# Kernel optimization log

Measured on AMD Instinct MI355X. Metric: run time of the kernel, lower is better.

## Reference

```python
import jax, jax.numpy as jnp
import numpy as np

B, T, D, H = 4, 2048, 512, 8
SCALE = np.float32(1.0 / np.sqrt(D))  # 'vaswani' scale, tied scalar, non-trainable
MASK_BIAS = np.float32(1e9)           # TF dense_attention masking constant


def setup_inputs() -> dict:
    key = jax.random.key(0)
    ks = jax.random.split(key, 5)
    s = 0.02  # small init so softmax logits are well-scaled
    return {
        "query": jax.random.normal(ks[0], (B, T, D), jnp.float32),
        "value": jax.random.normal(ks[1], (B, T, D), jnp.float32),
        "Wq": jax.random.normal(ks[2], (D, D * H), jnp.float32) * s,
        "bq": jnp.zeros((D * H,), jnp.float32),
        "Wk": jax.random.normal(ks[3], (D, D * H), jnp.float32) * s,
        "bk": jnp.zeros((D * H,), jnp.float32),
        "Wv": jax.random.normal(ks[4], (D, D * H), jnp.float32) * s,
        "bv": jnp.zeros((D * H,), jnp.float32),
    }


def reference(query, value, Wq, bq, Wk, bk, Wv, bv):
    # Per-head Dense projections (linear activation, depth=1): [B,T,D] -> [B,T,H*D]
    # split(axis=-1) into H heads + concat(axis=0) == reshape to [B,T,H,D]
    # (head h occupies contiguous slice [h*D:(h+1)*D] of the last axis)
    q = (query @ Wq + bq).reshape(B, T, H, D)
    k = (value @ Wk + bk).reshape(B, T, H, D)  # key defaults to value
    v = (value @ Wv + bv).reshape(B, T, H, D)
    # multiplicative scores: matmul(scale*q, k^T) -> [B,H,Tq,Tv]
    scores = jnp.einsum('bqhd,bkhd->bhqk', SCALE * q, k)
    # causal mask applied TF-style: scores -= 1e9 * (~mask)
    causal = jnp.tril(jnp.ones((T, T), bool))
    scores = jnp.where(causal, scores, scores - MASK_BIAS)
    attn = jax.nn.softmax(scores, axis=-1)          # [B,H,Tq,Tv]
    out = jnp.einsum('bhqk,bkhd->bqhd', attn, v)    # [B,Tq,H,D]
    # heads_output_mode='cat': concat heads back on feature axis
    return out.reshape(B, T, H * D)
```

## Files before the change

kernel.cpp:

```cpp
#include <hip/hip_runtime.h>
#include <stdint.h>

#define Bsz 4
#define Tsz 2048
#define Dsz 512
#define Hsz 8
#define HDsz 4096
#define Msz 8192
#define SCALE 0.044194173824159216f

typedef __attribute__((ext_vector_type(8))) short bf16x8;
typedef __attribute__((ext_vector_type(4))) float f32x4;
typedef __attribute__((ext_vector_type(4))) short s16x4;

static __device__ __forceinline__ short f2bf(float x) {
    uint32_t b = __float_as_uint(x);
    b += 0x7fff + ((b >> 16) & 1);
    return (short)(b >> 16);
}

__global__ __launch_bounds__(256) void xcast_kernel(
    const float* __restrict__ Xq, const float* __restrict__ Xv,
    short* __restrict__ Oq, short* __restrict__ Ov)
{
    int idx = blockIdx.x * 256 + threadIdx.x;
    const float* src = (idx < 1048576) ? Xq : Xv;
    short* dst = (idx < 1048576) ? Oq : Ov;
    int i = (idx < 1048576) ? idx : idx - 1048576;
    float4 v = *(const float4*)&src[(size_t)i * 4];
    s16x4 o;
    o.x = f2bf(v.x); o.y = f2bf(v.y); o.z = f2bf(v.z); o.w = f2bf(v.w);
    *(s16x4*)&dst[(size_t)i * 4] = o;
}

__global__ __launch_bounds__(256) void wtrans_kernel(
    const float* __restrict__ Wq, const float* __restrict__ Wk,
    const float* __restrict__ Wv, short* __restrict__ WtAll)
{
    const float* W = (blockIdx.z == 0) ? Wq : (blockIdx.z == 1) ? Wk : Wv;
    short* Wt = WtAll + (size_t)blockIdx.z * (size_t)HDsz * Dsz;
    __shared__ float tile[32][33];
    int tx = threadIdx.x, ty = threadIdx.y;
    int k0 = blockIdx.x * 32, n0 = blockIdx.y * 32;
    for (int i = 0; i < 4; i++)
        tile[ty + i * 8][tx] = W[(size_t)(k0 + ty + i * 8) * HDsz + n0 + tx];
    __syncthreads();
    for (int i = 0; i < 4; i++)
        Wt[(size_t)(n0 + ty + i * 8) * Dsz + k0 + tx] = f2bf(tile[tx][ty + i * 8]);
}

__global__ __launch_bounds__(256, 2) void proj_gemm_kernel(
    const short* __restrict__ Xqb, const short* __restrict__ Xvb,
    const short* __restrict__ WtAll, const float* __restrict__ bq,
    const float* __restrict__ bk, const float* __restrict__ bv,
    short* __restrict__ Qo, short* __restrict__ Ko, short* __restrict__ Vto)
{
    const int mode = blockIdx.z;
    const short* X = (mode == 0) ? Xqb : Xvb;
    const short* Wt = WtAll + (size_t)mode * (size_t)HDsz * Dsz;
    const float* bias = (mode == 0) ? bq : (mode == 1) ? bk : bv;
    const int m0 = blockIdx.x * 128, n0 = blockIdx.y * 128;

    __shared__ short Als[128 * 32];
    __shared__ short Bls[128 * 32];

    const int tid = threadIdx.x;
    const int lane = tid & 63, wave = tid >> 6;
    const int quad = lane >> 4, l16 = lane & 15;
    const int wm = wave >> 1, wn = wave & 1;

    const int dmarow = lane >> 2;
    const int dmachunk = (lane & 3) ^ ((lane >> 3) & 3);
    const int rdsw = (quad ^ ((l16 >> 1) & 3)) * 8;

    f32x4 acc[4][4];
    for (int i = 0; i < 4; i++)
        for (int j = 0; j < 4; j++)
            acc[i][j] = f32x4{0.f, 0.f, 0.f, 0.f};

    for (int ks = 0; ks < Dsz; ks += 32) {
        __syncthreads();
        for (int s = 0; s < 2; s++) {
            int c = wave * 2 + s;
            int row = c * 16 + dmarow;
            const short* ga = X + (size_t)(m0 + row) * Dsz + ks + dmachunk * 8;
            __builtin_amdgcn_global_load_lds(
                (const __attribute__((address_space(1))) void*)ga,
                (__attribute__((address_space(3))) void*)&Als[c * 512], 16, 0, 0);
            const short* gb = Wt + (size_t)(n0 + row) * Dsz + ks + dmachunk * 8;
            __builtin_amdgcn_global_load_lds(
                (const __attribute__((address_space(1))) void*)gb,
                (__attribute__((address_space(3))) void*)&Bls[c * 512], 16, 0, 0);
        }
        __syncthreads();
        bf16x8 af[4], bfr[4];
        for (int i = 0; i < 4; i++)
            af[i] = *(const bf16x8*)&Als[(wm * 64 + i * 16 + l16) * 32 + rdsw];
        for (int j = 0; j < 4; j++)
            bfr[j] = *(const bf16x8*)&Bls[(wn * 64 + j * 16 + l16) * 32 + rdsw];
        for (int i = 0; i < 4; i++)
            for (int j = 0; j < 4; j++)
                acc[i][j] = __builtin_amdgcn_mfma_f32_16x16x32_bf16(
                    af[i], bfr[j], acc[i][j], 0, 0, 0);
    }

    for (int i = 0; i < 4; i++) {
        for (int j = 0; j < 4; j++) {
            int n = n0 + wn * 64 + j * 16 + l16;
            int h = n >> 9, d = n & 511;
            float bb = bias[n];
            int mbase = m0 + wm * 64 + i * 16 + quad * 4;
            int b = mbase >> 11, t = mbase & 2047;
            if (mode == 2) {
                s16x4 o;
                o.x = f2bf(acc[i][j][0] + bb);
                o.y = f2bf(acc[i][j][1] + bb);
                o.z = f2bf(acc[i][j][2] + bb);
                o.w = f2bf(acc[i][j][3] + bb);
                *(s16x4*)&Vto[((size_t)(b * Hsz + h) * Dsz + d) * Tsz + t] = o;
            } else {
                short* O = (mode == 0) ? Qo : Ko;
                float sc = (mode == 0) ? SCALE : 1.0f;
                for (int r = 0; r < 4; r++) {
                    float v = (acc[i][j][r] + bb) * sc;
                    O[((size_t)(b * Hsz + h) * Tsz + (t + r)) * Dsz + d] = f2bf(v);
                }
            }
        }
    }
}

__global__ __launch_bounds__(512, 2) void attn_kernel(
    const short* __restrict__ Q, const short* __restrict__ K,
    const short* __restrict__ Vt, float* __restrict__ out)
{
    extern __shared__ short smem[];

    const int bid = blockIdx.x;
    const int qt = 15 - (bid >> 5);
    const int bh = bid & 31;
    const int q0 = qt * 128;
    const short* Qb = Q + (size_t)bh * Tsz * Dsz;
    const short* Kb = K + (size_t)bh * Tsz * Dsz;
    const short* Vb = Vt + (size_t)bh * Dsz * Tsz;

    const int tid = threadIdx.x;
    const int lane = tid & 63, wave = tid >> 6;
    const int quad = lane >> 4, l16 = lane & 15;
    const int qw = q0 + wave * 16;
    short* Pw = smem + 74240 + wave * (16 * 40);
    const int vrow = tid >> 2, vch = tid & 3;

    bf16x8 qf[16];
    for (int ks = 0; ks < 16; ks++)
        qf[ks] = *(const bf16x8*)&Qb[(size_t)(qw + l16) * Dsz + ks * 32 + quad * 8];

    f32x4 acc[32];
    for (int dt = 0; dt < 32; dt++) acc[dt] = f32x4{0.f, 0.f, 0.f, 0.f};
    float lacc[4] = {0.f, 0.f, 0.f, 0.f};

    {
        short* Ks0 = smem;
        short* Vs0 = smem + 33280;
        for (int i = 0; i < 4; i++) {
            int r = wave * 4 + i;
            const short* gp = Kb + (size_t)r * Dsz + lane * 8;
            __builtin_amdgcn_global_load_lds(
                (const __attribute__((address_space(1))) void*)gp,
                (__attribute__((address_space(3))) void*)&Ks0[r * 520], 16, 0, 0);
        }
        for (int p = 0; p < 4; p++) {
            int row = p * 128 + vrow;
            bf16x8 v = *(const bf16x8*)&Vb[(size_t)row * Tsz + vch * 8];
            *(bf16x8*)&Vs0[row * 40 + vch * 8] = v;
        }
    }
    __syncthreads();

    const int nkv = 4 * (qt + 1);
    for (int kt = 0; kt < nkv; kt++) {
        const int kv0 = kt * 32;
        short* Ksc = smem + (kt & 1) * 16640;
        short* Vsc = smem + 33280 + (kt & 1) * 20480;
        const bool pref = (kt + 1 < nkv);

        bf16x8 vreg[4];
        if (pref) {
            const int kvn = kv0 + 32;
            short* Ksn = smem + ((kt + 1) & 1) * 16640;
            for (int i = 0; i < 4; i++) {
                int r = wave * 4 + i;
                const short* gp = Kb + (size_t)(kvn + r) * Dsz + lane * 8;
                __builtin_amdgcn_global_load_lds(
                    (const __attribute__((address_space(1))) void*)gp,
                    (__attribute__((address_space(3))) void*)&Ksn[r * 520], 16, 0, 0);
            }
            for (int p = 0; p < 4; p++) {
                int row = p * 128 + vrow;
                vreg[p] = *(const bf16x8*)&Vb[(size_t)row * Tsz + kvn + vch * 8];
            }
        }

        if (kv0 <= qw + 15) {
            f32x4 s0 = f32x4{0.f, 0.f, 0.f, 0.f}, s1 = f32x4{0.f, 0.f, 0.f, 0.f};
            for (int ks = 0; ks < 16; ks++) {
                bf16x8 b0 = *(const bf16x8*)&Ksc[l16 * 520 + ks * 32 + quad * 8];
                bf16x8 b1 = *(const bf16x8*)&Ksc[(16 + l16) * 520 + ks * 32 + quad * 8];
                s0 = __builtin_amdgcn_mfma_f32_16x16x32_bf16(qf[ks], b0, s0, 0, 0, 0);
                s1 = __builtin_amdgcn_mfma_f32_16x16x32_bf16(qf[ks], b1, s1, 0, 0, 0);
            }
            bool full = (kv0 + 31 <= qw);
            for (int r = 0; r < 4; r++) {
                int rowg = qw + quad * 4 + r;
                float p0 = __expf(fminf(s0[r], 40.f));
                float p1 = __expf(fminf(s1[r], 40.f));
                if (!full) {
                    if (kv0 + l16 > rowg) p0 = 0.f;
                    if (kv0 + 16 + l16 > rowg) p1 = 0.f;
                }
                lacc[r] += p0 + p1;
                Pw[(quad * 4 + r) * 40 + l16] = f2bf(p0);
                Pw[(quad * 4 + r) * 40 + 16 + l16] = f2bf(p1);
            }
            bf16x8 pa = *(const bf16x8*)&Pw[l16 * 40 + quad * 8];
            for (int dt = 0; dt < 32; dt++) {
                bf16x8 vb = *(const bf16x8*)&Vsc[(dt * 16 + l16) * 40 + quad * 8];
                acc[dt] = __builtin_amdgcn_mfma_f32_16x16x32_bf16(pa, vb, acc[dt], 0, 0, 0);
            }
        }

        if (pref) {
            short* Vsn = smem + 33280 + ((kt + 1) & 1) * 20480;
            for (int p = 0; p < 4; p++) {
                int row = p * 128 + vrow;
                *(bf16x8*)&Vsn[row * 40 + vch * 8] = vreg[p];
            }
        }
        __syncthreads();
    }

    const int b = bh >> 3, h = bh & 7;
    float inv[4];
    for (int r = 0; r < 4; r++) {
        float l = lacc[r];
        l += __shfl_xor(l, 1);
        l += __shfl_xor(l, 2);
        l += __shfl_xor(l, 4);
        l += __shfl_xor(l, 8);
        inv[r] = 1.0f / l;
    }
    for (int dt = 0; dt < 32; dt++) {
        for (int r = 0; r < 4; r++) {
            int t = qw + quad * 4 + r;
            out[(size_t)(b * Tsz + t) * HDsz + h * Dsz + dt * 16 + l16] =
                acc[dt][r] * inv[r];
        }
    }
}

extern "C" void kernel_launch(void* const* d_in, const int* in_sizes, int n_in,
                              void* d_out, int out_size, void* d_ws, size_t ws_size,
                              hipStream_t stream) {
    const float* query = (const float*)d_in[0];
    const float* value = (const float*)d_in[1];
    const float* Wq = (const float*)d_in[2];
    const float* bq = (const float*)d_in[3];
    const float* Wk = (const float*)d_in[4];
    const float* bk = (const float*)d_in[5];
    const float* Wv = (const float*)d_in[6];
    const float* bv = (const float*)d_in[7];
    float* out = (float*)d_out;

    char* ws = (char*)d_ws;
    short* Wt  = (short*)ws;
    short* Xqb = (short*)(ws + 12582912);
    short* Xvb = (short*)(ws + 20971520);
    short* Qb  = (short*)(ws + 29360128);
    short* Kb  = (short*)(ws + 96468992);
    short* Vtb = (short*)(ws + 163577856);

    (void)hipFuncSetAttribute((const void*)attn_kernel,
                        hipFuncAttributeMaxDynamicSharedMemorySize, 158720);

    xcast_kernel<<<8192, 256, 0, stream>>>(query, value, Xqb, Xvb);
    wtrans_kernel<<<dim3(16, 128, 3), dim3(32, 8), 0, stream>>>(Wq, Wk, Wv, Wt);
    proj_gemm_kernel<<<dim3(64, 32, 3), 256, 0, stream>>>(
        Xqb, Xvb, Wt, bq, bk, bv, Qb, Kb, Vtb);
    attn_kernel<<<dim3(512), dim3(512), 158720, stream>>>(Qb, Kb, Vtb, out);
}
```

Before: 551.3 us.

## Double-buffer projection GEMM LDS loads and stage epilogue through shared memory

The projection GEMM now double-buffers its A/B tiles in LDS, prefetching the next K-slice with async global-to-LDS loads while MFMAs run on the current one, and uses one barrier per iteration instead of two. The epilogue writes bias-added bf16 results into a padded LDS tile and then emits coalesced 16-byte global stores, replacing scattered 2-byte stores for Q/K and 8-byte strided stores for V^T. LDS use grows to about 34KB per block, which may reduce occupancy. Only the projection kernel changes; the attention kernel, which likely dominates time, is untouched.

```diff
diff --git a/kernel.cpp b/kernel.cpp
--- a/kernel.cpp
+++ b/kernel.cpp
@@ -61,8 +61,7 @@
     const float* bias = (mode == 0) ? bq : (mode == 1) ? bk : bv;
     const int m0 = blockIdx.x * 128, n0 = blockIdx.y * 128;
 
-    __shared__ short Als[128 * 32];
-    __shared__ short Bls[128 * 32];
+    __shared__ short sm[17408];
 
     const int tid = threadIdx.x;
     const int lane = tid & 63, wave = tid >> 6;
@@ -78,54 +77,86 @@
         for (int j = 0; j < 4; j++)
             acc[i][j] = f32x4{0.f, 0.f, 0.f, 0.f};
 
-    for (int ks = 0; ks < Dsz; ks += 32) {
-        __syncthreads();
-        for (int s = 0; s < 2; s++) {
-            int c = wave * 2 + s;
-            int row = c * 16 + dmarow;
-            const short* ga = X + (size_t)(m0 + row) * Dsz + ks + dmachunk * 8;
-            __builtin_amdgcn_global_load_lds(
-                (const __attribute__((address_space(1))) void*)ga,
-                (__attribute__((address_space(3))) void*)&Als[c * 512], 16, 0, 0);
-            const short* gb = Wt + (size_t)(n0 + row) * Dsz + ks + dmachunk * 8;
-            __builtin_amdgcn_global_load_lds(
-                (const __attribute__((address_space(1))) void*)gb,
-                (__attribute__((address_space(3))) void*)&Bls[c * 512], 16, 0, 0);
-        }
-        __syncthreads();
+#define STAGE(ksv, bufsel) do {                                                  \
+        const int _ks = (ksv);                                                   \
+        short* _A = sm + (bufsel) * 4096;                                        \
+        short* _B = sm + 8192 + (bufsel) * 4096;                                 \
+        for (int s = 0; s < 2; s++) {                                            \
+            int c = wave * 2 + s;                                                \
+            int row = c * 16 + dmarow;                                           \
+            const short* ga = X + (size_t)(m0 + row) * Dsz + _ks + dmachunk * 8; \
+            __builtin_amdgcn_global_load_lds(                                    \
+                (const __attribute__((address_space(1))) void*)ga,               \
+                (__attribute__((address_space(3))) void*)&_A[c * 512], 16, 0, 0);\
+            const short* gb = Wt + (size_t)(n0 + row) * Dsz + _ks + dmachunk * 8;\
+            __builtin_amdgcn_global_load_lds(                                    \
+                (const __attribute__((address_space(1))) void*)gb,               \
+                (__attribute__((address_space(3))) void*)&_B[c * 512], 16, 0, 0);\
+        }                                                                        \
+    } while (0)
+
+    STAGE(0, 0);
+    __syncthreads();
+
+    for (int t = 0; t < 16; t++) {
+        const int cur = t & 1;
+        if (t < 15) STAGE((t + 1) * 32, cur ^ 1);
+        const short* Ac = sm + cur * 4096;
+        const short* Bc = sm + 8192 + cur * 4096;
         bf16x8 af[4], bfr[4];
         for (int i = 0; i < 4; i++)
-            af[i] = *(const bf16x8*)&Als[(wm * 64 + i * 16 + l16) * 32 + rdsw];
+            af[i] = *(const bf16x8*)&Ac[(wm * 64 + i * 16 + l16) * 32 + rdsw];
         for (int j = 0; j < 4; j++)
-            bfr[j] = *(const bf16x8*)&Bls[(wn * 64 + j * 16 + l16) * 32 + rdsw];
+            bfr[j] = *(const bf16x8*)&Bc[(wn * 64 + j * 16 + l16) * 32 + rdsw];
         for (int i = 0; i < 4; i++)
             for (int j = 0; j < 4; j++)
                 acc[i][j] = __builtin_amdgcn_mfma_f32_16x16x32_bf16(
                     af[i], bfr[j], acc[i][j], 0, 0, 0);
-    }
-
-    for (int i = 0; i < 4; i++) {
-        for (int j = 0; j < 4; j++) {
-            int n = n0 + wn * 64 + j * 16 + l16;
-            int h = n >> 9, d = n & 511;
-            float bb = bias[n];
-            int mbase = m0 + wm * 64 + i * 16 + quad * 4;
-            int b = mbase >> 11, t = mbase & 2047;
-            if (mode == 2) {
-                s16x4 o;
-                o.x = f2bf(acc[i][j][0] + bb);
-                o.y = f2bf(acc[i][j][1] + bb);
-                o.z = f2bf(acc[i][j][2] + bb);
-                o.w = f2bf(acc[i][j][3] + bb);
-                *(s16x4*)&Vto[((size_t)(b * Hsz + h) * Dsz + d) * Tsz + t] = o;
-            } else {
-                short* O = (mode == 0) ? Qo : Ko;
-                float sc = (mode == 0) ? SCALE : 1.0f;
-                for (int r = 0; r < 4; r++) {
-                    float v = (acc[i][j][r] + bb) * sc;
-                    O[((size_t)(b * Hsz + h) * Tsz + (t + r)) * Dsz + d] = f2bf(v);
-                }
-            }
+        __syncthreads();
+    }
+#undef STAGE
+
+    const int b = m0 >> 11, t0 = m0 & 2047;
+    const int h = n0 >> 9, d0 = n0 & 511;
+    const float scv = (mode == 0) ? SCALE : 1.0f;
+
+    if (mode == 2) {
+        for (int i = 0; i < 4; i++)
+            for (int j = 0; j < 4; j++) {
+                int c = wn * 64 + j * 16 + l16;
+                float bb = bias[n0 + c];
+                int rb = wm * 64 + i * 16 + quad * 4;
+                for (int r = 0; r < 4; r++)
+                    sm[c * 136 + rb + r] = f2bf(acc[i][j][r] + bb);
+            }
+    } else {
+        for (int i = 0; i < 4; i++)
+            for (int j = 0; j < 4; j++) {
+                int c = wn * 64 + j * 16 + l16;
+                float bb = bias[n0 + c];
+                int rb = wm * 64 + i * 16 + quad * 4;
+                for (int r = 0; r < 4; r++)
+                    sm[(rb + r) * 136 + c] = f2bf((acc[i][j][r] + bb) * scv);
+            }
+    }
+    __syncthreads();
+
+    if (mode == 2) {
+        size_t base = ((size_t)(b * Hsz + h) * Dsz + d0) * Tsz + t0;
+        for (int k = 0; k < 8; k++) {
+            int cid = k * 256 + tid;
+            int c = cid >> 4, r8 = (cid & 15) * 8;
+            *(bf16x8*)&Vto[base + (size_t)c * Tsz + r8] =
+                *(const bf16x8*)&sm[c * 136 + r8];
+        }
+    } else {
+        short* O = (mode == 0) ? Qo : Ko;
+        size_t base = ((size_t)(b * Hsz + h) * Tsz + t0) * Dsz + d0;
+        for (int k = 0; k < 8; k++) {
+            int cid = k * 256 + tid;
+            int r = cid >> 4, c8 = (cid & 15) * 8;
+            *(bf16x8*)&O[base + (size_t)r * Dsz + c8] =
+                *(const bf16x8*)&sm[r * 136 + c8];
         }
     }
 }
```

New measurement: 538.7 us. 2.3% less time.
